# Performance work log

Measured on AMD Instinct MI355X. Metric: run time of the kernel, lower is better.

The kernel has to match this reference:

```python
import jax, jax.numpy as jnp
import numpy as np

EPS = 1e-12

def setup_inputs() -> dict:
    key = jax.random.key(0)
    k1, k2, k3, k4 = jax.random.split(key, 4)
    N_TABLE, N_NODES, N_SAMP, D_IN, D_OUT = 200000, 50000, 32, 256, 256
    features = jax.random.normal(k1, (N_TABLE, D_IN), dtype=jnp.float32)
    node_idx = jax.random.randint(k2, (N_NODES,), 0, N_TABLE)
    neigh_idx = jax.random.randint(k3, (N_NODES, N_SAMP), 0, N_TABLE)
    W = jax.random.normal(k4, (D_IN, D_OUT), dtype=jnp.float32) / np.sqrt(D_IN)
    b = jnp.zeros((D_OUT,), dtype=jnp.float32)
    return {"node_idx": node_idx, "neigh_idx": neigh_idx, "features": features, "W": W, "b": b}

def reference(node_idx, neigh_idx, features, W, b):
    # MeanAggregator with self_loop: mean over sampled neighbors + the node itself
    n_samp = neigh_idx.shape[1]
    neigh_feats = features[neigh_idx]            # [N, S, D] gather
    self_feats = features[node_idx]              # [N, D]
    agg = (neigh_feats.sum(axis=1) + self_feats) / (n_samp + 1)  # [N, D]
    # Combine: linear -> ReLU activation -> L2 normalize
    out = jax.nn.relu(agg @ W + b)               # [N, D_out]
    norm = jnp.sqrt(jnp.sum(out * out, axis=-1, keepdims=True))
    out = out / jnp.maximum(norm, EPS)
    return out
```

## Files before the change

kernel.cpp:

```cpp
#include <hip/hip_runtime.h>
#include <hip/hip_bf16.h>

typedef __attribute__((ext_vector_type(8))) short short8;
typedef __attribute__((ext_vector_type(4))) float f32x4;

#define D_IN   256
#define D_OUT  256
#define NSAMP  32

static __device__ __forceinline__ unsigned short f2bf(float f) {
    unsigned int u = __builtin_bit_cast(unsigned int, f);
    u += 0x7fffu + ((u >> 16) & 1u);
    return (unsigned short)(u >> 16);
}

__global__ void wconv_kernel(const float* __restrict__ W,
                             unsigned short* __restrict__ wsw) {
    const int k = blockIdx.x;
    const int n = threadIdx.x;
    const float v = W[k * D_OUT + n];
    const int ks = k >> 5, kg = (k >> 3) & 3, j = k & 7;
    const int nf = n >> 4, c = n & 15;
    const int lane = kg * 16 + c;
    const int dst = ((ks * 16 + nf) * 64 + lane) * 8 + j;
    wsw[dst] = f2bf(v);
}

__global__ __launch_bounds__(256, 4) void gcn_fused_kernel(
        const int*  __restrict__ node_idx,
        const int*  __restrict__ neigh_idx,
        const float* __restrict__ features,
        const unsigned short* __restrict__ wsw,
        const float* __restrict__ bias,
        float* __restrict__ out,
        int n_nodes)
{
    __shared__ __attribute__((aligned(16))) unsigned char lds[64 * D_IN * 2];

    const int tid  = threadIdx.x;
    const int wv   = tid >> 6;
    const int lane = tid & 63;
    const int block_m0 = blockIdx.x * 64;

    const float scale = 1.0f / (float)(NSAMP + 1);
    for (int r = 0; r < 16; ++r) {
        const int row  = wv * 16 + r;
        const int node = block_m0 + row;
        float ax = 0.f, ay = 0.f, az = 0.f, aw = 0.f;
        if (node < n_nodes) {
            const int nb   = neigh_idx[node * NSAMP + (lane & 31)];
            const int self = node_idx[node];
            {
                const float4 v = *(const float4*)(features + (size_t)self * D_IN + lane * 4);
                ax += v.x; ay += v.y; az += v.z; aw += v.w;
            }
            #pragma unroll 8
            for (int s = 0; s < NSAMP; ++s) {
                const int idx = __shfl(nb, s, 64);
                const float4 v = *(const float4*)(features + (size_t)idx * D_IN + lane * 4);
                ax += v.x; ay += v.y; az += v.z; aw += v.w;
            }
            ax *= scale; ay *= scale; az *= scale; aw *= scale;
        }
        ushort4 pk;
        pk.x = f2bf(ax); pk.y = f2bf(ay); pk.z = f2bf(az); pk.w = f2bf(aw);
        unsigned int bo = (unsigned int)(row * 512 + lane * 8) ^ ((unsigned int)(row & 7) << 4);
        *(ushort4*)(&lds[bo]) = pk;
    }

    __syncthreads();

    f32x4 acc[16];
    #pragma unroll
    for (int i = 0; i < 16; ++i) acc[i] = (f32x4)(0.0f);

    const int arow = wv * 16 + (lane & 15);
    const int acol = (lane >> 4) * 16;
    const short8* __restrict__ wp = (const short8*)wsw;

    #pragma unroll
    for (int ks = 0; ks < 8; ++ks) {
        unsigned int bo = (unsigned int)(arow * 512 + ks * 64 + acol)
                        ^ ((unsigned int)(arow & 7) << 4);
        const short8 afrag = *(const short8*)(&lds[bo]);
        #pragma unroll
        for (int nf = 0; nf < 16; ++nf) {
            const short8 bfrag = wp[(ks * 16 + nf) * 64 + lane];
            acc[nf] = __builtin_amdgcn_mfma_f32_16x16x32_bf16(afrag, bfrag, acc[nf], 0, 0, 0);
        }
    }

    float p[4] = {0.f, 0.f, 0.f, 0.f};
    #pragma unroll
    for (int nf = 0; nf < 16; ++nf) {
        const float bv = bias[nf * 16 + (lane & 15)];
        #pragma unroll
        for (int j = 0; j < 4; ++j) {
            float v = acc[nf][j] + bv;
            v = fmaxf(v, 0.0f);
            acc[nf][j] = v;
            p[j] += v * v;
        }
    }
    #pragma unroll
    for (int m = 1; m < 16; m <<= 1) {
        p[0] += __shfl_xor(p[0], m, 64);
        p[1] += __shfl_xor(p[1], m, 64);
        p[2] += __shfl_xor(p[2], m, 64);
        p[3] += __shfl_xor(p[3], m, 64);
    }
    float inv[4];
    #pragma unroll
    for (int j = 0; j < 4; ++j)
        inv[j] = 1.0f / fmaxf(sqrtf(p[j]), 1e-12f);

    const int rbase = block_m0 + wv * 16 + (lane >> 4) * 4;
    const int c0 = lane & 15;
    #pragma unroll
    for (int j = 0; j < 4; ++j) {
        const int rg = rbase + j;
        if (rg < n_nodes) {
            #pragma unroll
            for (int nf = 0; nf < 16; ++nf)
                out[(size_t)rg * D_OUT + nf * 16 + c0] = acc[nf][j] * inv[j];
        }
    }
}

extern "C" void kernel_launch(void* const* d_in, const int* in_sizes, int n_in,
                              void* d_out, int out_size, void* d_ws, size_t ws_size,
                              hipStream_t stream) {
    const int*   node_idx  = (const int*)d_in[0];
    const int*   neigh_idx = (const int*)d_in[1];
    const float* features  = (const float*)d_in[2];
    const float* W         = (const float*)d_in[3];
    const float* bias      = (const float*)d_in[4];
    float*       out       = (float*)d_out;
    const int n_nodes = in_sizes[0];

    unsigned short* wsw = (unsigned short*)d_ws;

    hipLaunchKernelGGL(wconv_kernel, dim3(D_IN), dim3(D_OUT), 0, stream, W, wsw);

    const int nblocks = (n_nodes + 63) / 64;
    hipLaunchKernelGGL(gcn_fused_kernel, dim3(nblocks), dim3(256), 0, stream,
                       node_idx, neigh_idx, features, wsw, bias, out, n_nodes);
}
```

Measured before the change: 509.9 us.

## Project feature table through W first, then gather bf16 projected rows

Uses linearity of the mean to swap order: every table row is first multiplied by W into a bf16 projected table Y, then each node gathers and averages 33 rows of Y and applies bias, ReLU and L2 norm. The gather now reads 512 bytes per row instead of 1 KB of fp32 features, which targets the random-access gather traffic. In exchange it does a GEMM over all 200k table rows instead of 50k nodes, adds a 100 MB write and read of Y, and adds bf16 rounding on the projected values before summation. It falls back to the old fused kernel when the workspace is too small.

```diff
diff --git a/kernel.cpp b/kernel.cpp
--- a/kernel.cpp
+++ b/kernel.cpp
@@ -12,6 +12,17 @@
     unsigned int u = __builtin_bit_cast(unsigned int, f);
     u += 0x7fffu + ((u >> 16) & 1u);
     return (unsigned short)(u >> 16);
+}
+
+static __device__ __forceinline__ void accum8(float* a, uint4 v) {
+    a[0] += __builtin_bit_cast(float, v.x << 16);
+    a[1] += __builtin_bit_cast(float, v.x & 0xffff0000u);
+    a[2] += __builtin_bit_cast(float, v.y << 16);
+    a[3] += __builtin_bit_cast(float, v.y & 0xffff0000u);
+    a[4] += __builtin_bit_cast(float, v.z << 16);
+    a[5] += __builtin_bit_cast(float, v.z & 0xffff0000u);
+    a[6] += __builtin_bit_cast(float, v.w << 16);
+    a[7] += __builtin_bit_cast(float, v.w & 0xffff0000u);
 }
 
 __global__ void wconv_kernel(const float* __restrict__ W,
@@ -24,6 +35,127 @@
     const int lane = kg * 16 + c;
     const int dst = ((ks * 16 + nf) * 64 + lane) * 8 + j;
     wsw[dst] = f2bf(v);
+}
+
+__global__ __launch_bounds__(256, 4) void ygemm_kernel(
+        const float* __restrict__ feat,
+        const unsigned short* __restrict__ wsw,
+        unsigned short* __restrict__ Y,
+        int n_table)
+{
+    __shared__ __attribute__((aligned(16))) unsigned char lds[64 * 512];
+
+    const int tid  = threadIdx.x;
+    const int wv   = tid >> 6;
+    const int lane = tid & 63;
+    const int row0 = blockIdx.x * 64;
+
+    const int r = tid >> 2;
+    const int q = tid & 3;
+    #pragma unroll 4
+    for (int it = 0; it < 16; ++it) {
+        const int cidx = it * 4 + q;
+        const int grow = row0 + r;
+        float4 f = make_float4(0.f, 0.f, 0.f, 0.f);
+        if (grow < n_table)
+            f = *(const float4*)(feat + (size_t)grow * D_IN + cidx * 4);
+        ushort4 pk;
+        pk.x = f2bf(f.x); pk.y = f2bf(f.y); pk.z = f2bf(f.z); pk.w = f2bf(f.w);
+        unsigned int bo = (unsigned int)(r * 512 + cidx * 8) ^ ((unsigned int)(r & 7) << 4);
+        *(ushort4*)(&lds[bo]) = pk;
+    }
+    __syncthreads();
+
+    f32x4 acc[16];
+    #pragma unroll
+    for (int i = 0; i < 16; ++i) acc[i] = (f32x4)(0.0f);
+
+    const int arow = wv * 16 + (lane & 15);
+    const int acol = (lane >> 4) * 16;
+    const short8* __restrict__ wp = (const short8*)wsw;
+
+    #pragma unroll
+    for (int ks = 0; ks < 8; ++ks) {
+        unsigned int bo = (unsigned int)(arow * 512 + ks * 64 + acol)
+                        ^ ((unsigned int)(arow & 7) << 4);
+        const short8 afrag = *(const short8*)(&lds[bo]);
+        #pragma unroll
+        for (int nf = 0; nf < 16; ++nf) {
+            const short8 bfrag = wp[(ks * 16 + nf) * 64 + lane];
+            acc[nf] = __builtin_amdgcn_mfma_f32_16x16x32_bf16(afrag, bfrag, acc[nf], 0, 0, 0);
+        }
+    }
+
+    const int rbase = row0 + wv * 16 + (lane >> 4) * 4;
+    const int c0 = lane & 15;
+    #pragma unroll
+    for (int j = 0; j < 4; ++j) {
+        const int rg = rbase + j;
+        if (rg < n_table) {
+            #pragma unroll
+            for (int nf = 0; nf < 16; ++nf)
+                Y[(size_t)rg * D_OUT + nf * 16 + c0] = f2bf(acc[nf][j]);
+        }
+    }
+}
+
+__global__ __launch_bounds__(256) void gather_kernel(
+        const int*  __restrict__ node_idx,
+        const int*  __restrict__ neigh_idx,
+        const unsigned short* __restrict__ Y,
+        const float* __restrict__ bias,
+        float* __restrict__ out,
+        int n_nodes)
+{
+    const int tid  = threadIdx.x;
+    const int l    = tid & 31;
+    const int node = blockIdx.x * 8 + (tid >> 5);
+    const bool valid = node < n_nodes;
+
+    const int nb   = valid ? neigh_idx[node * NSAMP + l] : 0;
+    const int sidx = valid ? node_idx[node] : 0;
+
+    float a[8] = {0.f, 0.f, 0.f, 0.f, 0.f, 0.f, 0.f, 0.f};
+
+    #pragma unroll 8
+    for (int s = 0; s < NSAMP; ++s) {
+        const int idx = __shfl(nb, s, 32);
+        const uint4 v = *(const uint4*)(Y + (size_t)idx * D_OUT + l * 8);
+        accum8(a, v);
+    }
+    {
+        const uint4 v = *(const uint4*)(Y + (size_t)sidx * D_OUT + l * 8);
+        accum8(a, v);
+    }
+
+    const float sc = 1.0f / (float)(NSAMP + 1);
+    const float4 b0 = *(const float4*)(bias + l * 8);
+    const float4 b1 = *(const float4*)(bias + l * 8 + 4);
+    float o[8];
+    o[0] = fmaxf(a[0] * sc + b0.x, 0.f);
+    o[1] = fmaxf(a[1] * sc + b0.y, 0.f);
+    o[2] = fmaxf(a[2] * sc + b0.z, 0.f);
+    o[3] = fmaxf(a[3] * sc + b0.w, 0.f);
+    o[4] = fmaxf(a[4] * sc + b1.x, 0.f);
+    o[5] = fmaxf(a[5] * sc + b1.y, 0.f);
+    o[6] = fmaxf(a[6] * sc + b1.z, 0.f);
+    o[7] = fmaxf(a[7] * sc + b1.w, 0.f);
+
+    float p = 0.f;
+    #pragma unroll
+    for (int j = 0; j < 8; ++j) p += o[j] * o[j];
+    #pragma unroll
+    for (int m = 1; m < 32; m <<= 1) p += __shfl_xor(p, m, 64);
+    const float inv = 1.0f / fmaxf(sqrtf(p), 1e-12f);
+
+    if (valid) {
+        float4 s0, s1;
+        s0.x = o[0] * inv; s0.y = o[1] * inv; s0.z = o[2] * inv; s0.w = o[3] * inv;
+        s1.x = o[4] * inv; s1.y = o[5] * inv; s1.z = o[6] * inv; s1.w = o[7] * inv;
+        float* op = out + (size_t)node * D_OUT + l * 8;
+        *(float4*)op       = s0;
+        *(float4*)(op + 4) = s1;
+    }
 }
 
 __global__ __launch_bounds__(256, 4) void gcn_fused_kernel(
@@ -67,7 +199,6 @@
         unsigned int bo = (unsigned int)(row * 512 + lane * 8) ^ ((unsigned int)(row & 7) << 4);
         *(ushort4*)(&lds[bo]) = pk;
     }
-
     __syncthreads();
 
     f32x4 acc[16];
@@ -137,12 +268,25 @@
     const float* bias      = (const float*)d_in[4];
     float*       out       = (float*)d_out;
     const int n_nodes = in_sizes[0];
+    const int n_table = in_sizes[2] / D_IN;
 
     unsigned short* wsw = (unsigned short*)d_ws;
+    unsigned short* Y   = (unsigned short*)((char*)d_ws + 131072);
+
+    const size_t need = 131072 + (size_t)n_table * D_OUT * 2;
 
     hipLaunchKernelGGL(wconv_kernel, dim3(D_IN), dim3(D_OUT), 0, stream, W, wsw);
 
-    const int nblocks = (n_nodes + 63) / 64;
-    hipLaunchKernelGGL(gcn_fused_kernel, dim3(nblocks), dim3(256), 0, stream,
-                       node_idx, neigh_idx, features, wsw, bias, out, n_nodes);
-}
+    if (ws_size >= need) {
+        const int yblocks = (n_table + 63) / 64;
+        hipLaunchKernelGGL(ygemm_kernel, dim3(yblocks), dim3(256), 0, stream,
+                           features, wsw, Y, n_table);
+        const int gblocks = (n_nodes + 7) / 8;
+        hipLaunchKernelGGL(gather_kernel, dim3(gblocks), dim3(256), 0, stream,
+                           node_idx, neigh_idx, Y, bias, out, n_nodes);
+    } else {
+        const int nblocks = (n_nodes + 63) / 64;
+        hipLaunchKernelGGL(gcn_fused_kernel, dim3(nblocks), dim3(256), 0, stream,
+                           node_idx, neigh_idx, features, wsw, bias, out, n_nodes);
+    }
+}
```

Result: slower. 528.2 us (+3.6%).
